# Optimization experiments

Measured on AMD Instinct MI355X. Metric: run time of the kernel, lower is better.

## Reference

```python
import jax, jax.numpy as jnp
import numpy as np

B, L, D, H = 4, 2048, 1024, 16
HD = D // H  # head dim = 64


def setup_inputs() -> dict:
    key = jax.random.key(0)
    ks = jax.random.split(key, 8)
    std_qkv = np.sqrt(D + D // H).astype(np.float32)  # matches nn.init.normal_ std in source
    xav = np.sqrt(2.0 / (D + D)).astype(np.float32)   # xavier_normal_ for fc_out
    return {
        "query": jax.random.normal(ks[0], (B, L, D), dtype=jnp.float32),
        "key": jax.random.normal(ks[1], (B, L, D), dtype=jnp.float32),
        "value": jax.random.normal(ks[2], (B, L, D), dtype=jnp.float32),
        "Wq": jax.random.normal(ks[3], (D, D), dtype=jnp.float32) * std_qkv,
        "Wk": jax.random.normal(ks[4], (D, D), dtype=jnp.float32) * std_qkv,
        "Wv": jax.random.normal(ks[5], (D, D), dtype=jnp.float32) * std_qkv,
        "Wo": jax.random.normal(ks[6], (D, D), dtype=jnp.float32) * xav,
        "bo": jnp.zeros((D,), dtype=jnp.float32),
    }


def reference(query, key, value, Wq, Wk, Wv, Wo, bo):
    # Linear projections (torch Linear: x @ W.T), then split heads: b l (h k) -> b h l k
    def split_heads(x):
        b, l, _ = x.shape
        return x.reshape(b, l, H, HD).transpose(0, 2, 1, 3)

    q = split_heads(query @ Wq.T)   # [B,H,L,HD]
    k = split_heads(key @ Wk.T)     # [B,H,T,HD]
    v = split_heads(value @ Wv.T)   # [B,H,T,HD]

    scale = 1.0 / np.sqrt(HD).astype(np.float32)
    energy = jnp.einsum("bhlk,bhtk->bhlt", q, k) * scale  # [B,H,L,T]
    attention = jax.nn.softmax(energy, axis=3)
    out = jnp.einsum("bhlt,bhtv->bhlv", attention, v)     # [B,H,L,HD]
    # b h l v -> b l (h v)
    out = out.transpose(0, 2, 1, 3).reshape(B, L, D)
    out = out @ Wo.T + bo  # dropout_rate=0.0 -> identity
    return out, attention
```

## Files before the change

kernel.cpp:

```cpp
#include <hip/hip_runtime.h>
#include <math.h>

#define Bb 4
#define Ls 2048
#define Dd 1024
#define Hh 16
#define HDm 64
#define ML (Bb*Ls)

typedef double f64x4 __attribute__((ext_vector_type(4)));
typedef float  f32x4 __attribute__((ext_vector_type(4)));
typedef short  bf16x8 __attribute__((ext_vector_type(8)));
typedef unsigned int u32;
typedef unsigned short u16;

__device__ __forceinline__ void gload16(const void* g, void* l) {
  __builtin_amdgcn_global_load_lds(
      (const __attribute__((address_space(1))) u32*)g,
      (__attribute__((address_space(3))) u32*)l, 16, 0, 0);
}

__device__ __forceinline__ u16 f2bf(float f) {
  u32 u = __float_as_uint(f);
  u += 0x7FFFu + ((u >> 16) & 1u);
  return (u16)(u >> 16);
}

__global__ __launch_bounds__(256) void gemm_nt_mfma_f64(
    const float* __restrict__ A, const float* __restrict__ B,
    double* __restrict__ C, double outscale) {
  const int N = Dd, K = Dd;
  __shared__ float As[64][17];
  __shared__ float Bs[64][17];
  const int tid = threadIdx.x;
  const int lane = tid & 63;
  const int w = tid >> 6;
  const int lrow = lane & 15, lk = lane >> 4;
  const int bm = blockIdx.y * 64, bn = blockIdx.x * 64;
  const int sr = tid >> 4, sc = tid & 15;

  f64x4 acc[4] = {{0.,0.,0.,0.},{0.,0.,0.,0.},{0.,0.,0.,0.},{0.,0.,0.,0.}};

  for (int k0 = 0; k0 < K; k0 += 16) {
#pragma unroll
    for (int i = 0; i < 4; i++) {
      int r = sr + 16 * i;
      As[r][sc] = A[(size_t)(bm + r) * K + k0 + sc];
      Bs[r][sc] = B[(size_t)(bn + r) * K + k0 + sc];
    }
    __syncthreads();
#pragma unroll
    for (int t = 0; t < 4; t++) {
      double a = (double)As[16 * w + lrow][4 * t + lk];
#pragma unroll
      for (int j = 0; j < 4; j++) {
        double bb = (double)Bs[16 * j + lrow][4 * t + lk];
        acc[j] = __builtin_amdgcn_mfma_f64_16x16x4f64(a, bb, acc[j], 0, 0, 0);
      }
    }
    __syncthreads();
  }
#pragma unroll
  for (int j = 0; j < 4; j++)
#pragma unroll
    for (int d = 0; d < 4; d++) {
      size_t m = (size_t)(bm + 16 * w + 4 * d + lk);
      C[m * N + bn + 16 * j + lrow] = acc[j][d] * outscale;
    }
}

__global__ __launch_bounds__(256) void gemm_nt_mfma_f32(
    const float* __restrict__ A, const float* __restrict__ B,
    const float* __restrict__ bias, float* __restrict__ C) {
  const int N = Dd, K = Dd;
  __shared__ float As[64][17];
  __shared__ float Bs[64][17];
  const int tid = threadIdx.x;
  const int lane = tid & 63;
  const int w = tid >> 6;
  const int lrow = lane & 15, lk = lane >> 4;
  const int bm = blockIdx.y * 64, bn = blockIdx.x * 64;
  const int sr = tid >> 4, sc = tid & 15;

  f64x4 acc[4] = {{0.,0.,0.,0.},{0.,0.,0.,0.},{0.,0.,0.,0.},{0.,0.,0.,0.}};

  for (int k0 = 0; k0 < K; k0 += 16) {
#pragma unroll
    for (int i = 0; i < 4; i++) {
      int r = sr + 16 * i;
      As[r][sc] = A[(size_t)(bm + r) * K + k0 + sc];
      Bs[r][sc] = B[(size_t)(bn + r) * K + k0 + sc];
    }
    __syncthreads();
#pragma unroll
    for (int t = 0; t < 4; t++) {
      double a = (double)As[16 * w + lrow][4 * t + lk];
#pragma unroll
      for (int j = 0; j < 4; j++) {
        double bb = (double)Bs[16 * j + lrow][4 * t + lk];
        acc[j] = __builtin_amdgcn_mfma_f64_16x16x4f64(a, bb, acc[j], 0, 0, 0);
      }
    }
    __syncthreads();
  }
#pragma unroll
  for (int j = 0; j < 4; j++)
#pragma unroll
    for (int d = 0; d < 4; d++) {
      size_t m = (size_t)(bm + 16 * w + 4 * d + lk);
      int n = bn + 16 * j + lrow;
      float v = (float)acc[j][d];
      if (bias) v += bias[n];
      C[m * N + n] = v;
    }
}

__global__ __launch_bounds__(256) void gemm_nt_mfma_bf16o(
    const float* __restrict__ A, const float* __restrict__ B,
    u16* __restrict__ C) {
  const int N = Dd, K = Dd;
  __shared__ float As[64][17];
  __shared__ float Bs[64][17];
  const int tid = threadIdx.x;
  const int lane = tid & 63;
  const int w = tid >> 6;
  const int lrow = lane & 15, lk = lane >> 4;
  const int bm = blockIdx.y * 64, bn = blockIdx.x * 64;
  const int sr = tid >> 4, sc = tid & 15;

  f64x4 acc[4] = {{0.,0.,0.,0.},{0.,0.,0.,0.},{0.,0.,0.,0.},{0.,0.,0.,0.}};

  for (int k0 = 0; k0 < K; k0 += 16) {
#pragma unroll
    for (int i = 0; i < 4; i++) {
      int r = sr + 16 * i;
      As[r][sc] = A[(size_t)(bm + r) * K + k0 + sc];
      Bs[r][sc] = B[(size_t)(bn + r) * K + k0 + sc];
    }
    __syncthreads();
#pragma unroll
    for (int t = 0; t < 4; t++) {
      double a = (double)As[16 * w + lrow][4 * t + lk];
#pragma unroll
      for (int j = 0; j < 4; j++) {
        double bb = (double)Bs[16 * j + lrow][4 * t + lk];
        acc[j] = __builtin_amdgcn_mfma_f64_16x16x4f64(a, bb, acc[j], 0, 0, 0);
      }
    }
    __syncthreads();
  }
#pragma unroll
  for (int j = 0; j < 4; j++)
#pragma unroll
    for (int d = 0; d < 4; d++) {
      size_t m = (size_t)(bm + 16 * w + 4 * d + lk);
      C[m * N + bn + 16 * j + lrow] = f2bf((float)acc[j][d]);
    }
}

__global__ __launch_bounds__(256) void attn_flash(
    double* __restrict__ Qd, const double* __restrict__ Kd,
    const u16* __restrict__ Vf, float* __restrict__ attn,
    float* __restrict__ O) {
  __shared__ __align__(16) double Kbuf[2][32 * 64];
  __shared__ __align__(16) u16    Vb16[2][32 * 64];
  __shared__ __align__(16) u16    Pb[4][16 * 32];
  __shared__ __align__(16) float  Fs[4][16];

  const int tid = threadIdx.x;
  const int lane = tid & 63;
  const int w = tid >> 6;
  const int lrow = lane & 15;
  const int lk = lane >> 4;
  const int blk = blockIdx.x;
  const int qt = blk & 31;
  const int h = (blk >> 5) & 15;
  const int b = blk >> 9;
  const int l0 = qt * 64;

  const double* Qg = Qd + ((size_t)(b * Ls + l0)) * Dd + h * HDm;
  const double* Kg = Kd + ((size_t)b * Ls) * Dd + h * HDm;
  const u16*    Vg = Vf + ((size_t)b * Ls) * Dd + h * HDm;
  float* aout = attn + ((size_t)((b * Hh + h) * Ls + l0)) * Ls;

  double qreg[16];
#pragma unroll
  for (int t = 0; t < 16; t++)
    qreg[t] = Qg[(size_t)(16 * w + lrow) * Dd + 4 * t + lk];

  const int l16 = (lane & 31) * 16;
  const int halfk = lane >> 5;
  const int sx = (lrow & 7) << 1;

  auto stage = [&](int kts, int bsel) {
#pragma unroll
    for (int jj = 0; jj < 4; jj++) {
      int i = w + 4 * jj;
      int row = 2 * i + halfk;
      int inner = l16 ^ ((row & 7) << 4);
      const char* g = (const char*)Kg + (((size_t)(kts * 32 + row)) << 13) + inner;
      gload16(g, (char*)(&Kbuf[bsel][0]) + i * 1024);
    }
    {
      const char* g = (const char*)Vg +
          ((size_t)(kts * 32 + 8 * w + (lane >> 3))) * (Dd * 2) + (lane & 7) * 16;
      gload16(g, (char*)(&Vb16[bsel][0]) + w * 1024);
    }
  };

  float mreff[4];
  double sacc[4];
  f32x4 pacc[4];
#pragma unroll
  for (int d = 0; d < 4; d++) {
    mreff[d] = -INFINITY;
    sacc[d] = 0.0;
    pacc[d] = (f32x4){0.f, 0.f, 0.f, 0.f};
  }

  stage(0, 0);
  __syncthreads();

  int cur = 0;
  for (int kt = 0; kt < 64; kt++) {
    if (kt < 63) stage(kt + 1, cur ^ 1);

    const double* Kb = &Kbuf[cur][0];

    f64x4 acc0 = {0.0, 0.0, 0.0, 0.0};
    f64x4 acc1 = {0.0, 0.0, 0.0, 0.0};
#pragma unroll
    for (int t = 0; t < 16; t++) {
      int ko = (4 * t + lk) ^ sx;
      double b0 = Kb[lrow * 64 + ko];
      double b1 = Kb[(16 + lrow) * 64 + ko];
      acc0 = __builtin_amdgcn_mfma_f64_16x16x4f64(qreg[t], b0, acc0, 0, 0, 0);
      acc1 = __builtin_amdgcn_mfma_f64_16x16x4f64(qreg[t], b1, acc1, 0, 0, 0);
    }

#pragma unroll
    for (int d = 0; d < 4; d++) {
      double e0 = acc0[d];
      double e1 = acc1[d];
      float tmf = fmaxf((float)e0, (float)e1);
#pragma unroll
      for (int m = 1; m < 16; m <<= 1) tmf = fmaxf(tmf, __shfl_xor(tmf, m));
      float mo_f = mreff[d];
      float ref_f = fmaxf(mo_f, tmf);
      double ref = (double)ref_f;
      float p0 = expf((float)(e0 - ref));
      float p1 = expf((float)(e1 - ref));
      double ts = (double)p0 + (double)p1;
#pragma unroll
      for (int m = 1; m < 16; m <<= 1) ts += __shfl_xor(ts, m);
      float factor = expf(mo_f - ref_f);
      sacc[d] = sacc[d] * (double)factor + ts;
      mreff[d] = ref_f;
      int row = 16 * w + 4 * d + lk;
      aout[(size_t)row * Ls + kt * 32 + lrow] = p0;
      aout[(size_t)row * Ls + kt * 32 + 16 + lrow] = p1;
      if (lrow == 0) {
        ((float*)(Qd + ((size_t)(b * Ls + l0 + row)) * Dd + h * HDm))[kt] = ref_f;
        Fs[w][4 * d + lk] = factor;
      }
      Pb[w][(4 * d + lk) * 32 + lrow] = f2bf(p0);
      Pb[w][(4 * d + lk) * 32 + 16 + lrow] = f2bf(p1);
    }

    bf16x8 afr = *(const bf16x8*)&Pb[w][lrow * 32 + 8 * lk];
    f32x4 fv = *(const f32x4*)&Fs[w][4 * lk];
    const u16* Vb = &Vb16[cur][0];
#pragma unroll
    for (int q = 0; q < 4; q++) {
      pacc[q][0] *= fv[0];
      pacc[q][1] *= fv[1];
      pacc[q][2] *= fv[2];
      pacc[q][3] *= fv[3];
      bf16x8 bfr;
#pragma unroll
      for (int r = 0; r < 8; r++)
        bfr[r] = (short)Vb[(8 * lk + r) * 64 + 16 * q + lrow];
      pacc[q] = __builtin_amdgcn_mfma_f32_16x16x32_bf16(afr, bfr, pacc[q], 0, 0, 0);
    }

    __syncthreads();
    cur ^= 1;
  }

  if (lrow == 0) {
#pragma unroll
    for (int d = 0; d < 4; d++) Fs[w][4 * d + lk] = (float)(1.0 / sacc[d]);
  }
  f32x4 sv = *(const f32x4*)&Fs[w][4 * lk];
#pragma unroll
  for (int q = 0; q < 4; q++)
#pragma unroll
    for (int r = 0; r < 4; r++) {
      int row = 16 * w + 4 * lk + r;
      O[((size_t)(b * Ls + l0 + row)) * Dd + h * HDm + 16 * q + lrow] =
          pacc[q][r] * sv[r];
    }
  if (lrow == 0) {
#pragma unroll
    for (int d = 0; d < 4; d++) {
      int row = 16 * w + 4 * d + lk;
      float* mrow = (float*)(Qd + ((size_t)(b * Ls + l0 + row)) * Dd + h * HDm);
      mrow[64] = mreff[d];
      *(double*)(mrow + 66) = sacc[d];
    }
  }
}

__global__ __launch_bounds__(256) void attn_scale(
    float* __restrict__ attn, const double* __restrict__ Qd) {
  int R = blockIdx.x;
  int b = R >> 15;
  int rem = R & 32767;
  int h = rem >> 11;
  int l = rem & 2047;
  const float* mrow = (const float*)(Qd + ((size_t)(b * Ls + l)) * Dd + h * HDm);
  int tid = threadIdx.x;
  int kt = tid >> 2;
  double mt = (double)mrow[kt];
  double mf = (double)mrow[64];
  double s = *(const double*)(mrow + 66);
  float sc = (float)(exp(mt - mf) / s);
  float4* ap = (float4*)(attn + (size_t)R * Ls + tid * 8);
  float4 a0 = ap[0], a1 = ap[1];
  a0.x *= sc; a0.y *= sc; a0.z *= sc; a0.w *= sc;
  a1.x *= sc; a1.y *= sc; a1.z *= sc; a1.w *= sc;
  ap[0] = a0; ap[1] = a1;
}

extern "C" void kernel_launch(void* const* d_in, const int* in_sizes, int n_in,
                              void* d_out, int out_size, void* d_ws, size_t ws_size,
                              hipStream_t stream) {
  const float* query = (const float*)d_in[0];
  const float* key   = (const float*)d_in[1];
  const float* value = (const float*)d_in[2];
  const float* Wq    = (const float*)d_in[3];
  const float* Wk    = (const float*)d_in[4];
  const float* Wv    = (const float*)d_in[5];
  const float* Wo    = (const float*)d_in[6];
  const float* bo    = (const float*)d_in[7];

  float* out0 = (float*)d_out;
  float* attn = out0 + (size_t)ML * Dd;

  char* ws = (char*)d_ws;
  double* Qd  = (double*)ws;
  double* Kd  = (double*)(ws + (size_t)ML * Dd * 8);
  u16*    Vfb = (u16*)(ws + (size_t)ML * Dd * 16);
  float*  Of  = (float*)(ws + (size_t)ML * Dd * 16 + (size_t)ML * Dd * 2);

  dim3 gemm_grid(Dd / 64, ML / 64);
  gemm_nt_mfma_f64<<<gemm_grid, 256, 0, stream>>>(query, Wq, Qd, 0.125);
  gemm_nt_mfma_f64<<<gemm_grid, 256, 0, stream>>>(key,   Wk, Kd, 1.0);
  gemm_nt_mfma_bf16o<<<gemm_grid, 256, 0, stream>>>(value, Wv, Vfb);

  attn_flash<<<Bb * Hh * (Ls / 64), 256, 0, stream>>>(Qd, Kd, Vfb, attn, Of);
  attn_scale<<<Bb * Hh * Ls, 256, 0, stream>>>(attn, Qd);

  gemm_nt_mfma_f32<<<gemm_grid, 256, 0, stream>>>(Of, Wo, bo, out0);
}
```

Baseline: 3.972 ms.

## Double-buffer GEMM tiles with direct global-to-LDS loads and XOR swizzle

Moves the shared f64-MFMA GEMM mainloop into one helper used by the three projection kernels. Tiles are loaded with 16-byte global_load_lds straight into LDS and double-buffered, so the next K-slice loads while the current one computes, and one barrier per iteration replaces two. An XOR swizzle replaces the padded 17-column layout to avoid LDS bank conflicts. It doubles LDS use per block, and correctness depends on the swizzle matching the direct-to-LDS write pattern.

```diff
diff --git a/kernel.cpp b/kernel.cpp
--- a/kernel.cpp
+++ b/kernel.cpp
@@ -26,83 +26,82 @@
   return (u16)(u >> 16);
 }
 
+__device__ __forceinline__ void gemm_core_nt(
+    const float* __restrict__ A, const float* __restrict__ B,
+    int bm, int bn, int w, int lrow, int lk, f64x4 acc[4]) {
+  const int K = Dd;
+  __shared__ __align__(16) float As[2][64 * 16];
+  __shared__ __align__(16) float Bs[2][64 * 16];
+  const int tid = threadIdx.x;
+  const int r = tid >> 2, blk = tid & 3;
+  const int sblk = blk ^ ((r >> 1) & 3);
+  const int sxw = ((lrow >> 1) & 3) << 2;
+  const float* ga = A + (size_t)(bm + r) * K + 4 * sblk;
+  const float* gb = B + (size_t)(bn + r) * K + 4 * sblk;
+
+#pragma unroll
+  for (int j = 0; j < 4; j++) acc[j] = (f64x4){0., 0., 0., 0.};
+
+  char* la0 = (char*)&As[0][0] + w * 1024;
+  char* lb0 = (char*)&Bs[0][0] + w * 1024;
+  char* la1 = (char*)&As[1][0] + w * 1024;
+  char* lb1 = (char*)&Bs[1][0] + w * 1024;
+
+  gload16(ga, la0);
+  gload16(gb, lb0);
+  __syncthreads();
+
+  int cur = 0;
+  for (int k0 = 16; k0 <= K; k0 += 16) {
+    if (k0 < K) {
+      gload16(ga + k0, cur ? la0 : la1);
+      gload16(gb + k0, cur ? lb0 : lb1);
+    }
+    const float* Abuf = &As[cur][0];
+    const float* Bbuf = &Bs[cur][0];
+#pragma unroll
+    for (int t = 0; t < 4; t++) {
+      double a = (double)Abuf[(16 * w + lrow) * 16 + ((4 * t + lk) ^ sxw)];
+#pragma unroll
+      for (int j = 0; j < 4; j++) {
+        double bv = (double)Bbuf[(16 * j + lrow) * 16 + ((4 * t + lk) ^ sxw)];
+        acc[j] = __builtin_amdgcn_mfma_f64_16x16x4f64(a, bv, acc[j], 0, 0, 0);
+      }
+    }
+    __syncthreads();
+    cur ^= 1;
+  }
+}
+
 __global__ __launch_bounds__(256) void gemm_nt_mfma_f64(
     const float* __restrict__ A, const float* __restrict__ B,
     double* __restrict__ C, double outscale) {
-  const int N = Dd, K = Dd;
-  __shared__ float As[64][17];
-  __shared__ float Bs[64][17];
   const int tid = threadIdx.x;
   const int lane = tid & 63;
   const int w = tid >> 6;
   const int lrow = lane & 15, lk = lane >> 4;
   const int bm = blockIdx.y * 64, bn = blockIdx.x * 64;
-  const int sr = tid >> 4, sc = tid & 15;
-
-  f64x4 acc[4] = {{0.,0.,0.,0.},{0.,0.,0.,0.},{0.,0.,0.,0.},{0.,0.,0.,0.}};
-
-  for (int k0 = 0; k0 < K; k0 += 16) {
-#pragma unroll
-    for (int i = 0; i < 4; i++) {
-      int r = sr + 16 * i;
-      As[r][sc] = A[(size_t)(bm + r) * K + k0 + sc];
-      Bs[r][sc] = B[(size_t)(bn + r) * K + k0 + sc];
-    }
-    __syncthreads();
-#pragma unroll
-    for (int t = 0; t < 4; t++) {
-      double a = (double)As[16 * w + lrow][4 * t + lk];
-#pragma unroll
-      for (int j = 0; j < 4; j++) {
-        double bb = (double)Bs[16 * j + lrow][4 * t + lk];
-        acc[j] = __builtin_amdgcn_mfma_f64_16x16x4f64(a, bb, acc[j], 0, 0, 0);
-      }
-    }
-    __syncthreads();
-  }
+  f64x4 acc[4];
+  gemm_core_nt(A, B, bm, bn, w, lrow, lk, acc);
 #pragma unroll
   for (int j = 0; j < 4; j++)
 #pragma unroll
     for (int d = 0; d < 4; d++) {
       size_t m = (size_t)(bm + 16 * w + 4 * d + lk);
-      C[m * N + bn + 16 * j + lrow] = acc[j][d] * outscale;
+      C[m * Dd + bn + 16 * j + lrow] = acc[j][d] * outscale;
     }
 }
 
 __global__ __launch_bounds__(256) void gemm_nt_mfma_f32(
     const float* __restrict__ A, const float* __restrict__ B,
     const float* __restrict__ bias, float* __restrict__ C) {
-  const int N = Dd, K = Dd;
-  __shared__ float As[64][17];
-  __shared__ float Bs[64][17];
   const int tid = threadIdx.x;
   const int lane = tid & 63;
   const int w = tid >> 6;
   const int lrow = lane & 15, lk = lane >> 4;
   const int bm = blockIdx.y * 64, bn = blockIdx.x * 64;
-  const int sr = tid >> 4, sc = tid & 15;
-
-  f64x4 acc[4] = {{0.,0.,0.,0.},{0.,0.,0.,0.},{0.,0.,0.,0.},{0.,0.,0.,0.}};
-
-  for (int k0 = 0; k0 < K; k0 += 16) {
-#pragma unroll
-    for (int i = 0; i < 4; i++) {
-      int r = sr + 16 * i;
-      As[r][sc] = A[(size_t)(bm + r) * K + k0 + sc];
-      Bs[r][sc] = B[(size_t)(bn + r) * K + k0 + sc];
-    }
-    __syncthreads();
-#pragma unroll
-    for (int t = 0; t < 4; t++) {
-      double a = (double)As[16 * w + lrow][4 * t + lk];
-#pragma unroll
-      for (int j = 0; j < 4; j++) {
-        double bb = (double)Bs[16 * j + lrow][4 * t + lk];
-        acc[j] = __builtin_amdgcn_mfma_f64_16x16x4f64(a, bb, acc[j], 0, 0, 0);
-      }
-    }
-    __syncthreads();
-  }
+  f64x4 acc[4];
+  gemm_core_nt(A, B, bm, bn, w, lrow, lk, acc);
 #pragma unroll
   for (int j = 0; j < 4; j++)
 #pragma unroll
@@ -111,50 +110,26 @@
       int n = bn + 16 * j + lrow;
       float v = (float)acc[j][d];
       if (bias) v += bias[n];
-      C[m * N + n] = v;
+      C[m * Dd + n] = v;
     }
 }
 
 __global__ __launch_bounds__(256) void gemm_nt_mfma_bf16o(
     const float* __restrict__ A, const float* __restrict__ B,
     u16* __restrict__ C) {
-  const int N = Dd, K = Dd;
-  __shared__ float As[64][17];
-  __shared__ float Bs[64][17];
   const int tid = threadIdx.x;
   const int lane = tid & 63;
   const int w = tid >> 6;
   const int lrow = lane & 15, lk = lane >> 4;
   const int bm = blockIdx.y * 64, bn = blockIdx.x * 64;
-  const int sr = tid >> 4, sc = tid & 15;
-
-  f64x4 acc[4] = {{0.,0.,0.,0.},{0.,0.,0.,0.},{0.,0.,0.,0.},{0.,0.,0.,0.}};
-
-  for (int k0 = 0; k0 < K; k0 += 16) {
-#pragma unroll
-    for (int i = 0; i < 4; i++) {
-      int r = sr + 16 * i;
-      As[r][sc] = A[(size_t)(bm + r) * K + k0 + sc];
-      Bs[r][sc] = B[(size_t)(bn + r) * K + k0 + sc];
-    }
-    __syncthreads();
-#pragma unroll
-    for (int t = 0; t < 4; t++) {
-      double a = (double)As[16 * w + lrow][4 * t + lk];
-#pragma unroll
-      for (int j = 0; j < 4; j++) {
-        double bb = (double)Bs[16 * j + lrow][4 * t + lk];
-        acc[j] = __builtin_amdgcn_mfma_f64_16x16x4f64(a, bb, acc[j], 0, 0, 0);
-      }
-    }
-    __syncthreads();
-  }
+  f64x4 acc[4];
+  gemm_core_nt(A, B, bm, bn, w, lrow, lk, acc);
 #pragma unroll
   for (int j = 0; j < 4; j++)
 #pragma unroll
     for (int d = 0; d < 4; d++) {
       size_t m = (size_t)(bm + 16 * w + 4 * d + lk);
-      C[m * N + bn + 16 * j + lrow] = f2bf((float)acc[j][d]);
+      C[m * Dd + bn + 16 * j + lrow] = f2bf((float)acc[j][d]);
     }
 }
 
```

New measurement: 3.969 ms. No clear change (-0.1%).
